# Performance work log

Measured on AMD Instinct MI355X. Metric: run time of the kernel, lower is better.

The kernel has to match this reference:

```python
import jax, jax.numpy as jnp
import numpy as np

S, B, D, H, F, E = 2048, 8, 512, 8, 2048, 64
CAP_FACTOR = 2
EPS = 1e-5


def setup_inputs() -> dict:
    key = jax.random.key(0)
    ks = jax.random.split(key, 12)
    s = 0.02
    return {
        "src": jax.random.normal(ks[0], (S, B, D), jnp.float32),
        "in_proj_w": jax.random.normal(ks[1], (3 * D, D), jnp.float32) * s,
        "in_proj_b": jnp.zeros((3 * D,), jnp.float32),
        "out_proj_w": jax.random.normal(ks[2], (D, D), jnp.float32) * s,
        "out_proj_b": jnp.zeros((D,), jnp.float32),
        "ln1_g": jnp.ones((D,), jnp.float32),
        "ln1_b": jnp.zeros((D,), jnp.float32),
        "gate_w": jax.random.normal(ks[3], (D, E), jnp.float32) * s,
        "w1": jax.random.normal(ks[4], (E, D, F), jnp.float32) * s,
        "b1": jnp.zeros((E, F), jnp.float32),
        "w2": jax.random.normal(ks[5], (E, F, D), jnp.float32) * s,
        "b2": jnp.zeros((E, D), jnp.float32),
        "ln2_g": jnp.ones((D,), jnp.float32),
        "ln2_b": jnp.zeros((D,), jnp.float32),
    }


def _layer_norm(x, g, b):
    mu = jnp.mean(x, -1, keepdims=True)
    var = jnp.mean(jnp.square(x - mu), -1, keepdims=True)
    return (x - mu) * jax.lax.rsqrt(var + EPS) * g + b


def reference(src, in_proj_w, in_proj_b, out_proj_w, out_proj_b,
              ln1_g, ln1_b, gate_w, w1, b1, w2, b2, ln2_g, ln2_b):
    hd = D // H
    # --- self attention (seq-first, as nn.MultiheadAttention) ---
    qkv = src @ in_proj_w.T + in_proj_b            # [S,B,3D]
    q, k, v = jnp.split(qkv, 3, axis=-1)
    q = q.reshape(S, B, H, hd)
    k = k.reshape(S, B, H, hd)
    v = v.reshape(S, B, H, hd)
    scores = jnp.einsum('qbhd,kbhd->bhqk', q, k) * (hd ** -0.5)
    attn = jax.nn.softmax(scores, axis=-1)
    ctx = jnp.einsum('bhqk,kbhd->qbhd', attn, v).reshape(S, B, D)
    attn_out = ctx @ out_proj_w.T + out_proj_b
    x = _layer_norm(src + attn_out, ln1_g, ln1_b)

    # --- MoE: top-1 gating + capacity dispatch + merged expert FFN ---
    N = S * B
    C = CAP_FACTOR * N // E                         # per-expert capacity
    xt = x.reshape(N, D)
    probs = jax.nn.softmax(xt @ gate_w, axis=-1)    # [N,E]
    eidx = jnp.argmax(probs, axis=-1)               # [N]
    gval = jnp.take_along_axis(probs, eidx[:, None], 1)[:, 0]
    onehot = jax.nn.one_hot(eidx, E, dtype=jnp.int32)
    pos = jnp.take_along_axis(jnp.cumsum(onehot, 0), eidx[:, None], 1)[:, 0] - 1
    pos_s = jnp.where(pos < C, pos, C)              # overflow tokens -> dummy slot C
    buf = jnp.zeros((E, C + 1, D), xt.dtype).at[eidx, pos_s].set(xt)
    xe = buf[:, :C]                                 # [E,C,D]
    h = jax.nn.relu(jnp.einsum('ecd,edf->ecf', xe, w1) + b1[:, None, :])
    ye = jnp.einsum('ecf,efd->ecd', h, w2) + b2[:, None, :]
    ye = jnp.pad(ye, ((0, 0), (0, 1), (0, 0)))      # slot C = zeros (dropped)
    yt = ye[eidx, pos_s] * gval[:, None]            # combine with gate weight
    moe_out = yt.reshape(S, B, D)

    return _layer_norm(x + moe_out, ln2_g, ln2_b)
```

## Files before the change

kernel.cpp:

```cpp
#include <hip/hip_runtime.h>
#include <hip/hip_bf16.h>

typedef __bf16 bf16_t;
typedef __bf16 bf16x8 __attribute__((ext_vector_type(8)));
typedef float f32x4 __attribute__((ext_vector_type(4)));

static constexpr int S_ = 2048;
static constexpr int B_ = 8;
static constexpr int D_ = 512;
static constexpr int H_ = 8;
static constexpr int HD_ = 64;
static constexpr int F_ = 2048;
static constexpr int E_ = 64;
static constexpr int NT = S_ * B_;
static constexpr int CAP = 512;
static constexpr float EPS_ = 1e-5f;

__device__ __forceinline__ float wave_sum(float v) {
#pragma unroll
  for (int m = 1; m < 64; m <<= 1) v += __shfl_xor(v, m);
  return v;
}

__device__ __forceinline__ void gload_lds16(const void* g, void* l) {
  __builtin_amdgcn_global_load_lds((const __attribute__((address_space(1))) void*)g,
                                   (__attribute__((address_space(3))) void*)l, 16, 0, 0);
}

__device__ __forceinline__ unsigned pack2bf(float lo, float hi) {
  union { bf16_t h; unsigned short u; } a, b;
  a.h = (bf16_t)lo; b.h = (bf16_t)hi;
  return ((unsigned)b.u << 16) | (unsigned)a.u;
}

__global__ void k_cvt(const float* __restrict__ in, bf16_t* __restrict__ out, int n8) {
  int i = blockIdx.x * blockDim.x + threadIdx.x;
  if (i >= n8) return;
  const float4* p = (const float4*)in + (size_t)i * 2;
  float4 a = p[0], b = p[1];
  bf16x8 o;
  o[0]=(bf16_t)a.x; o[1]=(bf16_t)a.y; o[2]=(bf16_t)a.z; o[3]=(bf16_t)a.w;
  o[4]=(bf16_t)b.x; o[5]=(bf16_t)b.y; o[6]=(bf16_t)b.z; o[7]=(bf16_t)b.w;
  ((bf16x8*)out)[i] = o;
}

__global__ void k_tcvt(const float* __restrict__ in, bf16_t* __restrict__ out,
                       int R, int C, long strideIn, long strideOut) {
  __shared__ __align__(16) float t[64][68];
  const float* ip = in + (long)blockIdx.z * strideIn;
  bf16_t* op = out + (long)blockIdx.z * strideOut;
  int r0 = blockIdx.y * 64, c0 = blockIdx.x * 64;
  int tid = threadIdx.x;
  int row = tid >> 2, cc = (tid & 3) * 16;
  const float4* g = (const float4*)(ip + (long)(r0 + row) * C + c0 + cc);
  float4 a0 = g[0], a1 = g[1], a2 = g[2], a3 = g[3];
  *(float4*)&t[row][cc + 0]  = a0;
  *(float4*)&t[row][cc + 4]  = a1;
  *(float4*)&t[row][cc + 8]  = a2;
  *(float4*)&t[row][cc + 12] = a3;
  __syncthreads();
  int oc = tid >> 2, rr = (tid & 3) * 16;
  bf16x8 o0, o1;
#pragma unroll
  for (int j = 0; j < 8; j++) o0[j] = (bf16_t)t[rr + j][oc];
#pragma unroll
  for (int j = 0; j < 8; j++) o1[j] = (bf16_t)t[rr + 8 + j][oc];
  *(bf16x8*)(op + (long)(c0 + oc) * R + r0 + rr)     = o0;
  *(bf16x8*)(op + (long)(c0 + oc) * R + r0 + rr + 8) = o1;
}

__global__ void k_tv(const bf16_t* __restrict__ qkv, bf16_t* __restrict__ vT) {
  __shared__ __align__(16) bf16_t t[64][72];
  int bh = blockIdx.y, bI = bh >> 3, hI = bh & 7;
  int s0 = blockIdx.x * 64;
  int tid = threadIdx.x;
  int row = tid >> 2, cc = (tid & 3) * 16;
  const uint4* g = (const uint4*)(qkv + ((long)(s0 + row) * B_ + bI) * 1536 + 1024 + hI * 64 + cc);
  uint4 v0 = g[0], v1 = g[1];
  *(uint4*)&t[row][cc]     = v0;
  *(uint4*)&t[row][cc + 8] = v1;
  __syncthreads();
  int oc = tid >> 2, rr = (tid & 3) * 16;
  bf16x8 o0, o1;
#pragma unroll
  for (int j = 0; j < 8; j++) o0[j] = t[rr + j][oc];
#pragma unroll
  for (int j = 0; j < 8; j++) o1[j] = t[rr + 8 + j][oc];
  bf16_t* op = vT + ((long)bh * 64 + oc) * (long)S_ + s0 + rr;
  *(bf16x8*)(op)     = o0;
  *(bf16x8*)(op + 8) = o1;
}

template <int RELU>
__global__ __launch_bounds__(256) void k_gemm(
    const bf16_t* __restrict__ A, const bf16_t* __restrict__ Bm,
    const float* __restrict__ bias, bf16_t* __restrict__ Cout,
    int K, int lda, int ldb, int ldc,
    long aStride, long bStride, long cStride, int biasStride,
    const int* __restrict__ cnt, int mCap) {
  __shared__ __align__(16) bf16_t As[128 * 32];
  __shared__ __align__(16) bf16_t Bs[128 * 32];
  int z = blockIdx.z;
  if (cnt) {
    int c = cnt[z]; if (c > mCap) c = mCap;
    if ((int)blockIdx.y * 128 >= c) return;
  }
  long m0 = (long)blockIdx.y * 128, n0 = (long)blockIdx.x * 128;
  const bf16_t* Ab = A + (long)z * aStride + m0 * lda;
  const bf16_t* Bb = Bm + (long)z * bStride + n0 * ldb;
  int tid = threadIdx.x, wid = tid >> 6, lane = tid & 63;
  int lr = lane & 15, lg = lane >> 4;
  int wm = wid >> 1, wn = wid & 1;
  int grow = wid * 16 + (lane >> 2);
  int gcol = (lane & 3) * 8;
  const bf16_t* gA0 = Ab + (long)grow * lda + gcol;
  const bf16_t* gA1 = gA0 + (long)64 * lda;
  const bf16_t* gB0 = Bb + (long)grow * ldb + gcol;
  const bf16_t* gB1 = gB0 + (long)64 * ldb;
  bf16_t* lA0 = &As[wid * 512 + lane * 8];
  bf16_t* lA1 = lA0 + 2048;
  bf16_t* lB0 = &Bs[wid * 512 + lane * 8];
  bf16_t* lB1 = lB0 + 2048;
  f32x4 acc[4][4] = {};
  for (int k0 = 0; k0 < K; k0 += 32) {
    gload_lds16(gA0 + k0, lA0);
    gload_lds16(gA1 + k0, lA1);
    gload_lds16(gB0 + k0, lB0);
    gload_lds16(gB1 + k0, lB1);
    __syncthreads();
    bf16x8 af[4], bfr[4];
#pragma unroll
    for (int i = 0; i < 4; i++) {
      af[i]  = *(const bf16x8*)&As[(wm * 64 + i * 16 + lr) * 32 + lg * 8];
      bfr[i] = *(const bf16x8*)&Bs[(wn * 64 + i * 16 + lr) * 32 + lg * 8];
    }
#pragma unroll
    for (int i = 0; i < 4; i++)
#pragma unroll
      for (int j = 0; j < 4; j++)
        acc[i][j] = __builtin_amdgcn_mfma_f32_16x16x32_bf16(af[i], bfr[j], acc[i][j], 0, 0, 0);
    __syncthreads();
  }
#pragma unroll
  for (int j = 0; j < 4; j++) {
    int col = (int)n0 + wn * 64 + j * 16 + lr;
    float bv = bias[(long)z * biasStride + col];
#pragma unroll
    for (int i = 0; i < 4; i++) {
      long row = m0 + wm * 64 + i * 16 + lg * 4;
#pragma unroll
      for (int r = 0; r < 4; r++) {
        float v = acc[i][j][r] + bv;
        if (RELU) v = fmaxf(v, 0.0f);
        Cout[(long)z * cStride + (row + r) * ldc + col] = (bf16_t)v;
      }
    }
  }
}

__global__ __launch_bounds__(256) void k_attn(const bf16_t* __restrict__ qkv,
                                              const bf16_t* __restrict__ vT,
                                              bf16_t* __restrict__ ctx) {
  constexpr int LP = 80;
  __shared__ __align__(16) bf16_t Kld[64 * LP];
  __shared__ __align__(16) bf16_t Vld[64 * LP];
  int bh = blockIdx.y, bI = bh >> 3, hI = bh & 7;
  int q0 = blockIdx.x * 64;
  int tid = threadIdx.x, wid = tid >> 6, lane = tid & 63;
  int lr = lane & 15, lg = lane >> 4;
  int qrow = q0 + wid * 16 + lr;
  const bf16_t* qb = qkv + ((long)qrow * B_ + bI) * 1536 + hI * 64;
  bf16x8 qf0 = *(const bf16x8*)(qb + lg * 8);
  bf16x8 qf1 = *(const bf16x8*)(qb + 32 + lg * 8);
  f32x4 o[4] = {};
  float mrun = -3.0e38f, lrun = 0.0f;
  const float SC = 0.125f * 1.44269504f;
  int s0sh = lr + ((lane & 16) ? 32 : 0);
  int hi = lg >> 1;
  int srow = tid >> 2, sc = (tid & 3) * 16;
  for (int kb = 0; kb < S_ / 64; kb++) {
    int krow = kb * 64 + srow;
    const uint4* kg = (const uint4*)(qkv + ((long)krow * B_ + bI) * 1536 + 512 + hI * 64 + sc);
    const uint4* vg = (const uint4*)(vT + ((long)bh * 64 + srow) * (long)S_ + kb * 64 + sc);
    uint4 k0v = kg[0], k1v = kg[1], v0v = vg[0], v1v = vg[1];
    __syncthreads();
    *(uint4*)&Kld[srow * LP + sc]     = k0v;
    *(uint4*)&Kld[srow * LP + sc + 8] = k1v;
    *(uint4*)&Vld[srow * LP + sc]     = v0v;
    *(uint4*)&Vld[srow * LP + sc + 8] = v1v;
    __syncthreads();
    f32x4 sacc[4] = {};
#pragma unroll
    for (int kc = 0; kc < 2; kc++) {
      bf16x8 qf = kc ? qf1 : qf0;
#pragma unroll
      for (int kt = 0; kt < 4; kt++) {
        bf16x8 kf = *(const bf16x8*)&Kld[(kt * 16 + lr) * LP + kc * 32 + lg * 8];
        sacc[kt] = __builtin_amdgcn_mfma_f32_16x16x32_bf16(kf, qf, sacc[kt], 0, 0, 0);
      }
    }
#pragma unroll
    for (int kt = 0; kt < 4; kt++) sacc[kt] *= SC;
    float mx = -3.0e38f;
#pragma unroll
    for (int kt = 0; kt < 4; kt++)
#pragma unroll
      for (int r = 0; r < 4; r++) mx = fmaxf(mx, sacc[kt][r]);
    mx = fmaxf(mx, __shfl_xor(mx, 16));
    mx = fmaxf(mx, __shfl_xor(mx, 32));
    float mnew = fmaxf(mrun, mx);
    float corr = exp2f(mrun - mnew);
    mrun = mnew;
    float ps = 0.0f;
    unsigned pk[8];
#pragma unroll
    for (int kt = 0; kt < 4; kt++) {
      float p0 = exp2f(sacc[kt][0] - mnew);
      float p1 = exp2f(sacc[kt][1] - mnew);
      float p2 = exp2f(sacc[kt][2] - mnew);
      float p3 = exp2f(sacc[kt][3] - mnew);
      ps += (p0 + p1) + (p2 + p3);
      pk[kt * 2]     = pack2bf(p0, p1);
      pk[kt * 2 + 1] = pack2bf(p2, p3);
    }
    ps += __shfl_xor(ps, 16);
    ps += __shfl_xor(ps, 32);
    lrun = lrun * corr + ps;
    float cr[4];
#pragma unroll
    for (int r = 0; r < 4; r++) cr[r] = __shfl(corr, lg * 4 + r);
#pragma unroll
    for (int nt = 0; nt < 4; nt++)
#pragma unroll
      for (int r = 0; r < 4; r++) o[nt][r] *= cr[r];
#pragma unroll
    for (int ks = 0; ks < 2; ks++) {
      unsigned w[4];
#pragma unroll
      for (int h = 0; h < 2; h++) {
        unsigned vA = pk[4 * ks + h];
        unsigned vB = pk[4 * ks + 2 + h];
        unsigned a0 = (unsigned)__shfl((int)vA, s0sh);
        unsigned a1 = (unsigned)__shfl((int)vA, s0sh + 16);
        unsigned b0 = (unsigned)__shfl((int)vB, s0sh);
        unsigned b1 = (unsigned)__shfl((int)vB, s0sh + 16);
        w[h]     = hi ? b0 : a0;
        w[2 + h] = hi ? b1 : a1;
      }
      union { unsigned u[4]; bf16x8 v; } pw;
      pw.u[0] = w[0]; pw.u[1] = w[1]; pw.u[2] = w[2]; pw.u[3] = w[3];
#pragma unroll
      for (int nt = 0; nt < 4; nt++) {
        bf16x8 vb = *(const bf16x8*)&Vld[(nt * 16 + lr) * LP + ks * 32 + lg * 8];
        o[nt] = __builtin_amdgcn_mfma_f32_16x16x32_bf16(pw.v, vb, o[nt], 0, 0, 0);
      }
    }
  }
  float lr4[4];
#pragma unroll
  for (int r = 0; r < 4; r++) lr4[r] = __shfl(lrun, lg * 4 + r);
#pragma unroll
  for (int nt = 0; nt < 4; nt++)
#pragma unroll
    for (int r = 0; r < 4; r++) {
      int qr = q0 + wid * 16 + lg * 4 + r;
      float val = o[nt][r] / lr4[r];
      ctx[((long)qr * B_ + bI) * (long)D_ + hI * 64 + nt * 16 + lr] = (bf16_t)val;
    }
}

__global__ void k_ln_res(const float* __restrict__ base, const bf16_t* __restrict__ addb,
                         const float* __restrict__ g, const float* __restrict__ b,
                         float* __restrict__ out) {
  int w = (int)((blockIdx.x * blockDim.x + threadIdx.x) >> 6);
  int lane = threadIdx.x & 63;
  if (w >= NT) return;
  long off = (long)w * D_ + lane * 8;
  const float4* pb = (const float4*)(base + off);
  float4 b0 = pb[0], b1 = pb[1];
  bf16x8 av = *(const bf16x8*)(addb + off);
  float t[8];
  t[0]=b0.x+(float)av[0]; t[1]=b0.y+(float)av[1]; t[2]=b0.z+(float)av[2]; t[3]=b0.w+(float)av[3];
  t[4]=b1.x+(float)av[4]; t[5]=b1.y+(float)av[5]; t[6]=b1.z+(float)av[6]; t[7]=b1.w+(float)av[7];
  float s = t[0]+t[1]+t[2]+t[3]+t[4]+t[5]+t[6]+t[7];
  s = wave_sum(s);
  float mu = s * (1.0f / D_);
  float vv = 0.0f;
#pragma unroll
  for (int j = 0; j < 8; j++) { float d = t[j] - mu; vv += d * d; }
  vv = wave_sum(vv);
  float rstd = rsqrtf(vv * (1.0f / D_) + EPS_);
  const float4* pg = (const float4*)(g + lane * 8);
  const float4* pq = (const float4*)(b + lane * 8);
  float4 g0 = pg[0], g1 = pg[1], q0 = pq[0], q1 = pq[1];
  float4 o0, o1;
  o0.x=(t[0]-mu)*rstd*g0.x+q0.x; o0.y=(t[1]-mu)*rstd*g0.y+q0.y;
  o0.z=(t[2]-mu)*rstd*g0.z+q0.z; o0.w=(t[3]-mu)*rstd*g0.w+q0.w;
  o1.x=(t[4]-mu)*rstd*g1.x+q1.x; o1.y=(t[5]-mu)*rstd*g1.y+q1.y;
  o1.z=(t[6]-mu)*rstd*g1.z+q1.z; o1.w=(t[7]-mu)*rstd*g1.w+q1.w;
  float4* po = (float4*)(out + off);
  po[0] = o0; po[1] = o1;
}

__global__ void k_gate(const float* __restrict__ x, const float* __restrict__ gw,
                       int* __restrict__ eidx, float* __restrict__ gval) {
  int w = (int)((blockIdx.x * blockDim.x + threadIdx.x) >> 6);
  int lane = threadIdx.x & 63;
  if (w >= NT) return;
  const float* xr = x + (long)w * D_;
  float a0 = 0.0f, a1 = 0.0f, a2 = 0.0f, a3 = 0.0f;
#pragma unroll 4
  for (int k = 0; k < D_; k += 4) {
    a0 = fmaf(xr[k + 0], gw[(k + 0) * E_ + lane], a0);
    a1 = fmaf(xr[k + 1], gw[(k + 1) * E_ + lane], a1);
    a2 = fmaf(xr[k + 2], gw[(k + 2) * E_ + lane], a2);
    a3 = fmaf(xr[k + 3], gw[(k + 3) * E_ + lane], a3);
  }
  float acc = (a0 + a1) + (a2 + a3);
  float v = acc; int idx = lane;
#pragma unroll
  for (int m = 1; m < 64; m <<= 1) {
    float ov = __shfl_xor(v, m);
    int oi = __shfl_xor(idx, m);
    if (ov > v || (ov == v && oi < idx)) { v = ov; idx = oi; }
  }
  float s = __expf(acc - v);
  s = wave_sum(s);
  if (lane == 0) { eidx[w] = idx; gval[w] = 1.0f / s; }
}

__global__ void k_route(const float* __restrict__ x, const int* __restrict__ eidx,
                        int* __restrict__ pos, int* __restrict__ cnt,
                        bf16_t* __restrict__ xe) {
  int w = (int)((blockIdx.x * blockDim.x + threadIdx.x) >> 6);
  int lane = threadIdx.x & 63;
  if (w >= NT) return;
  int e = eidx[w];
  int p = 0;
  if (lane == 0) p = atomicAdd(&cnt[e], 1);
  p = __shfl(p, 0);
  if (lane == 0) pos[w] = p;
  if (p < CAP) {
    const float4* px = (const float4*)(x + (long)w * D_ + lane * 8);
    float4 a = px[0], b = px[1];
    bf16x8 o;
    o[0]=(bf16_t)a.x; o[1]=(bf16_t)a.y; o[2]=(bf16_t)a.z; o[3]=(bf16_t)a.w;
    o[4]=(bf16_t)b.x; o[5]=(bf16_t)b.y; o[6]=(bf16_t)b.z; o[7]=(bf16_t)b.w;
    *(bf16x8*)(xe + ((long)e * CAP + p) * D_ + lane * 8) = o;
  }
}

__global__ void k_final(const float* __restrict__ x, const bf16_t* __restrict__ ye,
                        const int* __restrict__ eidx, const int* __restrict__ pos,
                        const float* __restrict__ gval,
                        const float* __restrict__ g, const float* __restrict__ b,
                        float* __restrict__ out) {
  int w = (int)((blockIdx.x * blockDim.x + threadIdx.x) >> 6);
  int lane = threadIdx.x & 63;
  if (w >= NT) return;
  int e = eidx[w], p = pos[w];
  float gv = gval[w];
  long off = (long)w * D_ + lane * 8;
  const float4* px = (const float4*)(x + off);
  float4 x0 = px[0], x1 = px[1];
  float t[8] = {x0.x, x0.y, x0.z, x0.w, x1.x, x1.y, x1.z, x1.w};
  if (p < CAP) {
    bf16x8 yv = *(const bf16x8*)(ye + ((long)e * CAP + p) * D_ + lane * 8);
#pragma unroll
    for (int j = 0; j < 8; j++) t[j] += (float)yv[j] * gv;
  }
  float s = t[0]+t[1]+t[2]+t[3]+t[4]+t[5]+t[6]+t[7];
  s = wave_sum(s);
  float mu = s * (1.0f / D_);
  float vv = 0.0f;
#pragma unroll
  for (int j = 0; j < 8; j++) { float d = t[j] - mu; vv += d * d; }
  vv = wave_sum(vv);
  float rstd = rsqrtf(vv * (1.0f / D_) + EPS_);
  const float4* pg = (const float4*)(g + lane * 8);
  const float4* pq = (const float4*)(b + lane * 8);
  float4 g0 = pg[0], g1 = pg[1], q0 = pq[0], q1 = pq[1];
  float4 o0, o1;
  o0.x=(t[0]-mu)*rstd*g0.x+q0.x; o0.y=(t[1]-mu)*rstd*g0.y+q0.y;
  o0.z=(t[2]-mu)*rstd*g0.z+q0.z; o0.w=(t[3]-mu)*rstd*g0.w+q0.w;
  o1.x=(t[4]-mu)*rstd*g1.x+q1.x; o1.y=(t[5]-mu)*rstd*g1.y+q1.y;
  o1.z=(t[6]-mu)*rstd*g1.z+q1.z; o1.w=(t[7]-mu)*rstd*g1.w+q1.w;
  float4* po = (float4*)(out + off);
  po[0] = o0; po[1] = o1;
}

extern "C" void kernel_launch(void* const* d_in, const int* in_sizes, int n_in,
                              void* d_out, int out_size, void* d_ws, size_t ws_size,
                              hipStream_t stream) {
  const float* src        = (const float*)d_in[0];
  const float* in_proj_w  = (const float*)d_in[1];
  const float* in_proj_b  = (const float*)d_in[2];
  const float* out_proj_w = (const float*)d_in[3];
  const float* out_proj_b = (const float*)d_in[4];
  const float* ln1_g      = (const float*)d_in[5];
  const float* ln1_b      = (const float*)d_in[6];
  const float* gate_w     = (const float*)d_in[7];
  const float* w1         = (const float*)d_in[8];
  const float* b1         = (const float*)d_in[9];
  const float* w2         = (const float*)d_in[10];
  const float* b2         = (const float*)d_in[11];
  const float* ln2_g      = (const float*)d_in[12];
  const float* ln2_b      = (const float*)d_in[13];
  (void)in_sizes; (void)n_in; (void)out_size; (void)ws_size;

  char* ws = (char*)d_ws;
  size_t off = 0;
  auto alloc = [&](size_t bytes) -> char* {
    char* p = ws + off; off += (bytes + 255) & ~(size_t)255; return p;
  };
  bf16_t* src_bf  = (bf16_t*)alloc((size_t)NT * D_ * 2);
  bf16_t* w_in_bf = (bf16_t*)alloc((size_t)3 * D_ * D_ * 2);
  bf16_t* w_out_bf= (bf16_t*)alloc((size_t)D_ * D_ * 2);
  bf16_t* qkv_bf  = (bf16_t*)alloc((size_t)NT * 3 * D_ * 2);
  bf16_t* vT      = (bf16_t*)alloc((size_t)B_ * H_ * HD_ * S_ * 2);
  bf16_t* ctx_bf  = (bf16_t*)alloc((size_t)NT * D_ * 2);
  bf16_t* ao_bf   = (bf16_t*)alloc((size_t)NT * D_ * 2);
  float*  x_f32   = (float*)alloc((size_t)NT * D_ * 4);
  bf16_t* w1t     = (bf16_t*)alloc((size_t)E_ * D_ * F_ * 2);
  bf16_t* w2t     = (bf16_t*)alloc((size_t)E_ * F_ * D_ * 2);
  bf16_t* xe      = (bf16_t*)alloc((size_t)E_ * CAP * D_ * 2);
  bf16_t* hbuf    = (bf16_t*)alloc((size_t)E_ * CAP * F_ * 2);
  bf16_t* ye      = (bf16_t*)alloc((size_t)E_ * CAP * D_ * 2);
  int*    eidx    = (int*)alloc((size_t)NT * 4);
  int*    pos     = (int*)alloc((size_t)NT * 4);
  float*  gval    = (float*)alloc((size_t)NT * 4);
  int*    cnt     = (int*)alloc((size_t)E_ * 4);

  k_cvt<<<NT * D_ / 8 / 256, 256, 0, stream>>>(src, src_bf, NT * D_ / 8);
  k_cvt<<<3 * D_ * D_ / 8 / 256, 256, 0, stream>>>(in_proj_w, w_in_bf, 3 * D_ * D_ / 8);
  k_cvt<<<D_ * D_ / 8 / 256, 256, 0, stream>>>(out_proj_w, w_out_bf, D_ * D_ / 8);
  k_tcvt<<<dim3(F_ / 64, D_ / 64, E_), 256, 0, stream>>>(w1, w1t, D_, F_, (long)D_ * F_, (long)D_ * F_);
  k_tcvt<<<dim3(D_ / 64, F_ / 64, E_), 256, 0, stream>>>(w2, w2t, F_, D_, (long)F_ * D_, (long)F_ * D_);

  k_gemm<0><<<dim3(12, 128, 1), 256, 0, stream>>>(src_bf, w_in_bf, in_proj_b, qkv_bf,
      512, 512, 512, 1536, 0, 0, 0, 0, nullptr, NT);

  k_tv<<<dim3(S_ / 64, B_ * H_), 256, 0, stream>>>(qkv_bf, vT);
  k_attn<<<dim3(S_ / 64, B_ * H_), 256, 0, stream>>>(qkv_bf, vT, ctx_bf);
  k_gemm<0><<<dim3(4, 128, 1), 256, 0, stream>>>(ctx_bf, w_out_bf, out_proj_b, ao_bf,
      512, 512, 512, 512, 0, 0, 0, 0, nullptr, NT);
  k_ln_res<<<NT / 4, 256, 0, stream>>>(src, ao_bf, ln1_g, ln1_b, x_f32);

  k_gate<<<NT / 4, 256, 0, stream>>>(x_f32, gate_w, eidx, gval);
  hipMemsetAsync(cnt, 0, E_ * 4, stream);
  hipMemsetAsync(xe, 0, (size_t)E_ * CAP * D_ * 2, stream);
  k_route<<<NT / 4, 256, 0, stream>>>(x_f32, eidx, pos, cnt, xe);

  k_gemm<1><<<dim3(F_ / 128, CAP / 128, E_), 256, 0, stream>>>(xe, w1t, b1, hbuf,
      512, 512, 512, 2048, (long)CAP * D_, (long)F_ * D_, (long)CAP * F_, F_, cnt, CAP);
  k_gemm<0><<<dim3(D_ / 128, CAP / 128, E_), 256, 0, stream>>>(hbuf, w2t, b2, ye,
      2048, 2048, 2048, 512, (long)CAP * F_, (long)F_ * D_, (long)CAP * D_, D_, cnt, CAP);

  k_final<<<NT / 4, 256, 0, stream>>>(x_f32, ye, eidx, pos, gval, ln2_g, ln2_b, (float*)d_out);
}
```

Before: 1.338 ms.

## Rework weight transpose, lazy softmax rescale, batched gating, bf16 routing copy

Several independent changes. The weight transpose-convert kernel now uses coalesced row loads with a padded LDS tile that avoids bank conflicts. The attention kernel only rescales its running max and accumulators when some lane's max grows by more than a threshold, which removes most rescale shuffles and multiplies. Gating processes four tokens per wave so each gate-weight load is reused, and LN1 also writes a bf16 copy of x so routing copies half the bytes. The cost is an extra bf16 write of x and a lazy-rescale bound that relies on exp2 staying within range.

```diff
diff --git a/kernel.cpp b/kernel.cpp
--- a/kernel.cpp
+++ b/kernel.cpp
@@ -46,27 +46,28 @@
 
 __global__ void k_tcvt(const float* __restrict__ in, bf16_t* __restrict__ out,
                        int R, int C, long strideIn, long strideOut) {
-  __shared__ __align__(16) float t[64][68];
+  __shared__ float t[64][65];
   const float* ip = in + (long)blockIdx.z * strideIn;
   bf16_t* op = out + (long)blockIdx.z * strideOut;
   int r0 = blockIdx.y * 64, c0 = blockIdx.x * 64;
   int tid = threadIdx.x;
-  int row = tid >> 2, cc = (tid & 3) * 16;
-  const float4* g = (const float4*)(ip + (long)(r0 + row) * C + c0 + cc);
-  float4 a0 = g[0], a1 = g[1], a2 = g[2], a3 = g[3];
-  *(float4*)&t[row][cc + 0]  = a0;
-  *(float4*)&t[row][cc + 4]  = a1;
-  *(float4*)&t[row][cc + 8]  = a2;
-  *(float4*)&t[row][cc + 12] = a3;
+  int lrow = tid >> 4, lch = tid & 15;
+#pragma unroll
+  for (int i = 0; i < 4; i++) {
+    int row = lrow + i * 16;
+    float4 v = *(const float4*)(ip + (long)(r0 + row) * C + c0 + lch * 4);
+    *(float4*)&t[row][lch * 4] = v;
+  }
   __syncthreads();
-  int oc = tid >> 2, rr = (tid & 3) * 16;
-  bf16x8 o0, o1;
-#pragma unroll
-  for (int j = 0; j < 8; j++) o0[j] = (bf16_t)t[rr + j][oc];
-#pragma unroll
-  for (int j = 0; j < 8; j++) o1[j] = (bf16_t)t[rr + 8 + j][oc];
-  *(bf16x8*)(op + (long)(c0 + oc) * R + r0 + rr)     = o0;
-  *(bf16x8*)(op + (long)(c0 + oc) * R + r0 + rr + 8) = o1;
+  int scrow = tid >> 3, sch = tid & 7;
+#pragma unroll
+  for (int i = 0; i < 2; i++) {
+    int c = scrow + i * 32;
+    bf16x8 o;
+#pragma unroll
+    for (int j = 0; j < 8; j++) o[j] = (bf16_t)t[sch * 8 + j][c];
+    *(bf16x8*)(op + (long)(c0 + c) * R + r0 + sch * 8) = o;
+  }
 }
 
 __global__ void k_tv(const bf16_t* __restrict__ qkv, bf16_t* __restrict__ vT) {
@@ -208,31 +209,34 @@
       for (int r = 0; r < 4; r++) mx = fmaxf(mx, sacc[kt][r]);
     mx = fmaxf(mx, __shfl_xor(mx, 16));
     mx = fmaxf(mx, __shfl_xor(mx, 32));
-    float mnew = fmaxf(mrun, mx);
-    float corr = exp2f(mrun - mnew);
-    mrun = mnew;
+    if (__any(mx > mrun + 8.0f)) {
+      float mnew = fmaxf(mrun, mx);
+      float corr = exp2f(mrun - mnew);
+      mrun = mnew;
+      lrun *= corr;
+      float cr[4];
+#pragma unroll
+      for (int r = 0; r < 4; r++) cr[r] = __shfl(corr, lg * 4 + r);
+#pragma unroll
+      for (int nt = 0; nt < 4; nt++)
+#pragma unroll
+        for (int r = 0; r < 4; r++) o[nt][r] *= cr[r];
+    }
     float ps = 0.0f;
     unsigned pk[8];
 #pragma unroll
     for (int kt = 0; kt < 4; kt++) {
-      float p0 = exp2f(sacc[kt][0] - mnew);
-      float p1 = exp2f(sacc[kt][1] - mnew);
-      float p2 = exp2f(sacc[kt][2] - mnew);
-      float p3 = exp2f(sacc[kt][3] - mnew);
+      float p0 = exp2f(sacc[kt][0] - mrun);
+      float p1 = exp2f(sacc[kt][1] - mrun);
+      float p2 = exp2f(sacc[kt][2] - mrun);
+      float p3 = exp2f(sacc[kt][3] - mrun);
       ps += (p0 + p1) + (p2 + p3);
       pk[kt * 2]     = pack2bf(p0, p1);
       pk[kt * 2 + 1] = pack2bf(p2, p3);
     }
     ps += __shfl_xor(ps, 16);
     ps += __shfl_xor(ps, 32);
-    lrun = lrun * corr + ps;
-    float cr[4];
-#pragma unroll
-    for (int r = 0; r < 4; r++) cr[r] = __shfl(corr, lg * 4 + r);
-#pragma unroll
-    for (int nt = 0; nt < 4; nt++)
-#pragma unroll
-      for (int r = 0; r < 4; r++) o[nt][r] *= cr[r];
+    lrun += ps;
 #pragma unroll
     for (int ks = 0; ks < 2; ks++) {
       unsigned w[4];
@@ -271,7 +275,7 @@
 
 __global__ void k_ln_res(const float* __restrict__ base, const bf16_t* __restrict__ addb,
                          const float* __restrict__ g, const float* __restrict__ b,
-                         float* __restrict__ out) {
+                         float* __restrict__ out, bf16_t* __restrict__ outb) {
   int w = (int)((blockIdx.x * blockDim.x + threadIdx.x) >> 6);
   int lane = threadIdx.x & 63;
   if (w >= NT) return;
@@ -300,36 +304,49 @@
   o1.z=(t[6]-mu)*rstd*g1.z+q1.z; o1.w=(t[7]-mu)*rstd*g1.w+q1.w;
   float4* po = (float4*)(out + off);
   po[0] = o0; po[1] = o1;
+  bf16x8 xb;
+  xb[0]=(bf16_t)o0.x; xb[1]=(bf16_t)o0.y; xb[2]=(bf16_t)o0.z; xb[3]=(bf16_t)o0.w;
+  xb[4]=(bf16_t)o1.x; xb[5]=(bf16_t)o1.y; xb[6]=(bf16_t)o1.z; xb[7]=(bf16_t)o1.w;
+  *(bf16x8*)(outb + off) = xb;
 }
 
 __global__ void k_gate(const float* __restrict__ x, const float* __restrict__ gw,
                        int* __restrict__ eidx, float* __restrict__ gval) {
   int w = (int)((blockIdx.x * blockDim.x + threadIdx.x) >> 6);
   int lane = threadIdx.x & 63;
-  if (w >= NT) return;
-  const float* xr = x + (long)w * D_;
-  float a0 = 0.0f, a1 = 0.0f, a2 = 0.0f, a3 = 0.0f;
-#pragma unroll 4
+  if (w >= NT / 4) return;
+  const float* xr = x + (long)w * 4 * D_;
+  float a[4][4] = {};
   for (int k = 0; k < D_; k += 4) {
-    a0 = fmaf(xr[k + 0], gw[(k + 0) * E_ + lane], a0);
-    a1 = fmaf(xr[k + 1], gw[(k + 1) * E_ + lane], a1);
-    a2 = fmaf(xr[k + 2], gw[(k + 2) * E_ + lane], a2);
-    a3 = fmaf(xr[k + 3], gw[(k + 3) * E_ + lane], a3);
-  }
-  float acc = (a0 + a1) + (a2 + a3);
-  float v = acc; int idx = lane;
-#pragma unroll
-  for (int m = 1; m < 64; m <<= 1) {
-    float ov = __shfl_xor(v, m);
-    int oi = __shfl_xor(idx, m);
-    if (ov > v || (ov == v && oi < idx)) { v = ov; idx = oi; }
-  }
-  float s = __expf(acc - v);
-  s = wave_sum(s);
-  if (lane == 0) { eidx[w] = idx; gval[w] = 1.0f / s; }
-}
-
-__global__ void k_route(const float* __restrict__ x, const int* __restrict__ eidx,
+    float g0 = gw[(k + 0) * E_ + lane];
+    float g1 = gw[(k + 1) * E_ + lane];
+    float g2 = gw[(k + 2) * E_ + lane];
+    float g3 = gw[(k + 3) * E_ + lane];
+#pragma unroll
+    for (int tk = 0; tk < 4; tk++) {
+      const float* xt = xr + tk * D_;
+      a[tk][0] = fmaf(xt[k + 0], g0, a[tk][0]);
+      a[tk][1] = fmaf(xt[k + 1], g1, a[tk][1]);
+      a[tk][2] = fmaf(xt[k + 2], g2, a[tk][2]);
+      a[tk][3] = fmaf(xt[k + 3], g3, a[tk][3]);
+    }
+  }
+#pragma unroll
+  for (int tk = 0; tk < 4; tk++) {
+    float acc = (a[tk][0] + a[tk][1]) + (a[tk][2] + a[tk][3]);
+    float v = acc; int idx = lane;
+#pragma unroll
+    for (int m = 1; m < 64; m <<= 1) {
+      float ov = __shfl_xor(v, m);
+      int oi = __shfl_xor(idx, m);
+      if (ov > v || (ov == v && oi < idx)) { v = ov; idx = oi; }
+    }
+    float s = wave_sum(__expf(acc - v));
+    if (lane == 0) { eidx[w * 4 + tk] = idx; gval[w * 4 + tk] = 1.0f / s; }
+  }
+}
+
+__global__ void k_route(const bf16_t* __restrict__ xbf, const int* __restrict__ eidx,
                         int* __restrict__ pos, int* __restrict__ cnt,
                         bf16_t* __restrict__ xe) {
   int w = (int)((blockIdx.x * blockDim.x + threadIdx.x) >> 6);
@@ -341,11 +358,7 @@
   p = __shfl(p, 0);
   if (lane == 0) pos[w] = p;
   if (p < CAP) {
-    const float4* px = (const float4*)(x + (long)w * D_ + lane * 8);
-    float4 a = px[0], b = px[1];
-    bf16x8 o;
-    o[0]=(bf16_t)a.x; o[1]=(bf16_t)a.y; o[2]=(bf16_t)a.z; o[3]=(bf16_t)a.w;
-    o[4]=(bf16_t)b.x; o[5]=(bf16_t)b.y; o[6]=(bf16_t)b.z; o[7]=(bf16_t)b.w;
+    bf16x8 o = *(const bf16x8*)(xbf + (long)w * D_ + lane * 8);
     *(bf16x8*)(xe + ((long)e * CAP + p) * D_ + lane * 8) = o;
   }
 }
@@ -421,6 +434,7 @@
   bf16_t* ctx_bf  = (bf16_t*)alloc((size_t)NT * D_ * 2);
   bf16_t* ao_bf   = (bf16_t*)alloc((size_t)NT * D_ * 2);
   float*  x_f32   = (float*)alloc((size_t)NT * D_ * 4);
+  bf16_t* x_bf    = (bf16_t*)alloc((size_t)NT * D_ * 2);
   bf16_t* w1t     = (bf16_t*)alloc((size_t)E_ * D_ * F_ * 2);
   bf16_t* w2t     = (bf16_t*)alloc((size_t)E_ * F_ * D_ * 2);
   bf16_t* xe      = (bf16_t*)alloc((size_t)E_ * CAP * D_ * 2);
@@ -444,12 +458,12 @@
   k_attn<<<dim3(S_ / 64, B_ * H_), 256, 0, stream>>>(qkv_bf, vT, ctx_bf);
   k_gemm<0><<<dim3(4, 128, 1), 256, 0, stream>>>(ctx_bf, w_out_bf, out_proj_b, ao_bf,
       512, 512, 512, 512, 0, 0, 0, 0, nullptr, NT);
-  k_ln_res<<<NT / 4, 256, 0, stream>>>(src, ao_bf, ln1_g, ln1_b, x_f32);
-
-  k_gate<<<NT / 4, 256, 0, stream>>>(x_f32, gate_w, eidx, gval);
+  k_ln_res<<<NT / 4, 256, 0, stream>>>(src, ao_bf, ln1_g, ln1_b, x_f32, x_bf);
+
+  k_gate<<<NT / 4 / 4, 256, 0, stream>>>(x_f32, gate_w, eidx, gval);
   hipMemsetAsync(cnt, 0, E_ * 4, stream);
   hipMemsetAsync(xe, 0, (size_t)E_ * CAP * D_ * 2, stream);
-  k_route<<<NT / 4, 256, 0, stream>>>(x_f32, eidx, pos, cnt, xe);
+  k_route<<<NT / 4, 256, 0, stream>>>(x_bf, eidx, pos, cnt, xe);
 
   k_gemm<1><<<dim3(F_ / 128, CAP / 128, E_), 256, 0, stream>>>(xe, w1t, b1, hbuf,
       512, 512, 512, 2048, (long)CAP * D_, (long)F_ * D_, (long)CAP * F_, F_, cnt, CAP);
```

New measurement: 1.298 ms. 1.03x faster.
